# Kernel optimization log

Measured on AMD Instinct MI355X. Metric: run time of the kernel, lower is better.

The kernel has to match this reference:

```python
import jax, jax.numpy as jnp
import numpy as np

B = 512          # number of (query, corpus) pairs
MAX_SET = 128    # max_set_size
D_IN, E_IN = 32, 16
D = 128          # node_state_dim == filters_3
E_ENC = 64
M_HID = 256
T_DIM = 128      # transform_dim
N_PROP = 5
SINKHORN_ITERS = 20
TEMP = 0.1
DEG = 8


def setup_inputs() -> dict:
    key = jax.random.key(0)
    ks = jax.random.split(key, 16)
    # alternating graph sizes: query 128/64, corpus 64/128
    qsizes = np.where(np.arange(B) % 2 == 0, 128, 64).astype(np.int32)
    csizes = np.where(np.arange(B) % 2 == 0, 64, 128).astype(np.int32)
    sizes_flat = np.stack([qsizes, csizes], 1).reshape(-1)        # [2B] interleaved q,c
    N = int(sizes_flat.sum())                                     # 98304
    E = DEG * N                                                   # 786432
    starts = np.concatenate([[0], np.cumsum(sizes_flat)[:-1]])
    graph_idx = np.repeat(np.arange(2 * B), sizes_flat).astype(np.int32)
    rng = np.random.default_rng(0)
    from_idx = rng.integers(0, N, E).astype(np.int64)
    g = graph_idx[from_idx]                                       # keep edges within a graph
    to_idx = (starts[g] + rng.integers(0, 1 << 30, E) % sizes_flat[g]).astype(np.int64)

    def W(k, shape):
        s = 1.0 / np.sqrt(shape[0])
        return jax.random.uniform(k, shape, jnp.float32, -s, s)

    return dict(
        node_features=jax.random.normal(ks[0], (N, D_IN), jnp.float32),
        edge_features=jax.random.normal(ks[1], (E, E_IN), jnp.float32),
        enc_node_w=W(ks[2], (D_IN, D)), enc_node_b=jnp.zeros((D,), jnp.float32),
        enc_edge_w=W(ks[3], (E_IN, E_ENC)), enc_edge_b=jnp.zeros((E_ENC,), jnp.float32),
        msg_w1=W(ks[4], (2 * D + E_ENC, M_HID)), msg_b1=jnp.zeros((M_HID,), jnp.float32),
        msg_w2=W(ks[5], (M_HID, D)), msg_b2=jnp.zeros((D,), jnp.float32),
        rmsg_w1=W(ks[6], (2 * D + E_ENC, M_HID)), rmsg_b1=jnp.zeros((M_HID,), jnp.float32),
        rmsg_w2=W(ks[7], (M_HID, D)), rmsg_b2=jnp.zeros((D,), jnp.float32),
        upd_w1=W(ks[8], (2 * D, M_HID)), upd_b1=jnp.zeros((M_HID,), jnp.float32),
        upd_w2=W(ks[9], (M_HID, D)), upd_b2=jnp.zeros((D,), jnp.float32),
        fc1_w=W(ks[10], (D, T_DIM)), fc1_b=jnp.zeros((T_DIM,), jnp.float32),
        fc2_w=W(ks[11], (T_DIM, T_DIM)), fc2_b=jnp.zeros((T_DIM,), jnp.float32),
        from_idx=jnp.asarray(from_idx, jnp.int32),
        to_idx=jnp.asarray(to_idx, jnp.int32),
        graph_idx=jnp.asarray(graph_idx, jnp.int32),
        qsizes=jnp.asarray(qsizes, jnp.int32),
        csizes=jnp.asarray(csizes, jnp.int32),
    )


def _mlp2(x, w1, b1, w2, b2):
    return jax.nn.relu(x @ w1 + b1) @ w2 + b2


def reference(node_features, edge_features, enc_node_w, enc_node_b, enc_edge_w, enc_edge_b,
              msg_w1, msg_b1, msg_w2, msg_b2, rmsg_w1, rmsg_b1, rmsg_w2, rmsg_b2,
              upd_w1, upd_b1, upd_w2, upd_b2, fc1_w, fc1_b, fc2_w, fc2_b,
              from_idx, to_idx, graph_idx, qsizes, csizes):
    N = node_features.shape[0]
    # GraphEncoder: linear MLPs on node / edge features
    h = node_features @ enc_node_w + enc_node_b                   # [N, D]
    e = edge_features @ enc_edge_w + enc_edge_b                   # [E, E_ENC]
    # GraphPropLayer applied n_prop_layers times (shared params)
    for _ in range(N_PROP):
        src, dst = h[from_idx], h[to_idx]
        m = _mlp2(jnp.concatenate([src, dst, e], -1), msg_w1, msg_b1, msg_w2, msg_b2)
        agg = jax.ops.segment_sum(m, to_idx, num_segments=N)
        mr = _mlp2(jnp.concatenate([dst, src, e], -1), rmsg_w1, rmsg_b1, rmsg_w2, rmsg_b2)
        agg = agg + jax.ops.segment_sum(mr, from_idx, num_segments=N)
        h = h + _mlp2(jnp.concatenate([agg, h], -1), upd_w1, upd_b1, upd_w2, upd_b2)
    # split into per-graph chunks and pad to MAX_SET (scatter by (pair, side, position))
    sizes_flat = jnp.stack([qsizes, csizes], 1).reshape(-1)       # [2B]
    starts = jnp.concatenate([jnp.zeros((1,), sizes_flat.dtype), jnp.cumsum(sizes_flat)[:-1]])
    pos = jnp.arange(N, dtype=jnp.int32) - starts[graph_idx]
    pair, side = graph_idx // 2, graph_idx % 2
    stacked = jnp.zeros((B, 2, MAX_SET, D), h.dtype).at[pair, side, pos].set(h)
    stacked_q, stacked_c = stacked[:, 0], stacked[:, 1]           # [B, MAX_SET, D]
    # masked transform
    tq = _mlp2(stacked_q, fc1_w, fc1_b, fc2_w, fc2_b)
    tc = _mlp2(stacked_c, fc1_w, fc1_b, fc2_w, fc2_b)
    ar = jnp.arange(MAX_SET)
    qmask = (ar[None, :] < qsizes[:, None]).astype(h.dtype)[:, :, None]
    cmask = (ar[None, :] < csizes[:, None]).astype(h.dtype)[:, :, None]
    mq, mc = qmask * tq, cmask * tc
    # sinkhorn (noise_factor = 0, temperature = 0.1, 20 iters)
    log_alpha = jnp.einsum('bqd,bcd->bqc', mq, mc) / TEMP         # [B, MAX_SET, MAX_SET]
    for _ in range(SINKHORN_ITERS):
        log_alpha = log_alpha - jax.scipy.special.logsumexp(log_alpha, axis=2, keepdims=True)
        log_alpha = log_alpha - jax.scipy.special.logsumexp(log_alpha, axis=1, keepdims=True)
    plan = jnp.exp(log_alpha)
    # masked residual score
    scores = -jnp.sum(jax.nn.relu(stacked_q - plan @ stacked_c), axis=(1, 2))  # [B]
    return scores
```

## Files before the change

kernel.cpp:

```cpp
#include <hip/hip_runtime.h>

using bf16x8 = __attribute__((ext_vector_type(8))) __bf16;
using u16x8  = __attribute__((ext_vector_type(8))) unsigned short;
using f32x4  = __attribute__((ext_vector_type(4))) float;
using f32x2  = __attribute__((ext_vector_type(2))) float;

#define DEV static __device__ __forceinline__

constexpr int NN = 98304;
constexpr int NE = 786432;
constexpr int NB = 512;

constexpr size_t OFF_HB  = 0;
constexpr size_t OFF_AGG = OFF_HB + (size_t)NN*128*2;
constexpr size_t OFF_TH  = OFF_AGG;
constexpr size_t OFF_TL  = OFF_AGG + (size_t)NN*128*2;
constexpr size_t OFF_W   = OFF_AGG + (size_t)NN*128*4;

constexpr size_t WO_W1TM = 0;
constexpr size_t WO_W1TR = WO_W1TM + (size_t)81920*2;
constexpr size_t WO_W2TM = WO_W1TR + (size_t)81920*2;
constexpr size_t WO_W2TR = WO_W2TM + (size_t)32768*2;
constexpr size_t WO_W1TU = WO_W2TR + (size_t)32768*2;
constexpr size_t WO_W2TU = WO_W1TU + (size_t)65536*2;
constexpr size_t WO_WNT  = WO_W2TU + (size_t)32768*2;
constexpr size_t WO_WETP = WO_WNT  + (size_t)4096*2;
constexpr size_t WO_FC1F = WO_WETP + (size_t)2048*2;
constexpr size_t WO_FC2F = WO_FC1F + (size_t)16384*4;
constexpr size_t WO_BNF  = WO_FC2F + (size_t)16384*4;
constexpr size_t WO_BEF  = WO_BNF + 128*4;
constexpr size_t WO_B1M  = WO_BEF + 64*4;
constexpr size_t WO_B2M  = WO_B1M + 256*4;
constexpr size_t WO_B1R  = WO_B2M + 128*4;
constexpr size_t WO_B2R  = WO_B1R + 256*4;
constexpr size_t WO_B1U  = WO_B2R + 128*4;
constexpr size_t WO_B2U  = WO_B1U + 256*4;
constexpr size_t WO_FC1B = WO_B2U + 128*4;
constexpr size_t WO_FC2B = WO_FC1B + 128*4;
constexpr size_t WO_FLAG = WO_FC2B + 128*4;
constexpr size_t WO_END  = WO_FLAG + 16;

constexpr size_t OFF_HL  = OFF_W + WO_END;
constexpr size_t WS_MINI = OFF_HL;
constexpr size_t WS_FULL = OFF_HL + (size_t)NN*128*2;

constexpr int    SCAN_CHUNKS= NN/256;
constexpr size_t CSR_INTS   = (size_t)2*(NN+1) + (size_t)2*NN + (size_t)2*NE + 768;
constexpr size_t CSR_BYTES  = CSR_INTS*4;
constexpr size_t WS_FULL_G  = WS_FULL + CSR_BYTES;
constexpr size_t WS_MINI_G  = WS_MINI + CSR_BYTES;

DEV unsigned short f2bf(float f){
  unsigned u = __float_as_uint(f);
  u += 0x7fffu + ((u >> 16) & 1u);
  return (unsigned short)(u >> 16);
}
DEV float bf2f(unsigned short s){ return __uint_as_float(((unsigned)s) << 16); }

DEV unsigned short ldbf(const void* p, size_t i, int fl){
  return fl ? ((const unsigned short*)p)[i] : f2bf(((const float*)p)[i]);
}
DEV float ldf(const void* p, size_t i, int fl){
  return fl ? bf2f(((const unsigned short*)p)[i]) : ((const float*)p)[i];
}

DEV f32x4 mfma16(u16x8 a, u16x8 b, f32x4 c){
  bf16x8 A, B;
  __builtin_memcpy(&A, &a, 16);
  __builtin_memcpy(&B, &b, 16);
  return __builtin_amdgcn_mfma_f32_16x16x32_bf16(A, B, c, 0, 0, 0);
}

__global__ void k_dtype(const unsigned short* nf_u16, int* flag){
  if (threadIdx.x != 0 || blockIdx.x != 0) return;
  int sane = 0;
  for (int i = 0; i < 64; ++i){
    unsigned short v = nf_u16[2*i];
    int e = (v >> 7) & 0xFF;
    if (e >= 0x70 && e <= 0x8E) sane++;
  }
  *flag = (sane >= 32) ? 1 : 0;
}

__global__ void k_sent(float* out){
  int i = blockIdx.x*256 + threadIdx.x;
  if (i < NB) out[i] = 10000.f;
}

__global__ void k_canary(void* out, const int* flag){
  int i = blockIdx.x*256 + threadIdx.x;
  if (i < NB){
    if (*flag) ((unsigned short*)out)[i] = (unsigned short)0x4580u;
    else       ((float*)out)[i] = 4096.f;
  }
}

__global__ void k_zero(float* agg){
  f32x4* p = (f32x4*)agg;
  int gtid = blockIdx.x*256 + threadIdx.x;
  for (int i = gtid; i < NN*128/4; i += 786432){
    f32x4 z = {0.f, 0.f, 0.f, 0.f};
    p[i] = z;
  }
}

__global__ void k_prep(
  const void* enc_node_w, const void* enc_node_b,
  const void* enc_edge_w, const void* enc_edge_b,
  const void* msg_w1, const void* msg_b1,
  const void* msg_w2, const void* msg_b2,
  const void* rmsg_w1, const void* rmsg_b1,
  const void* rmsg_w2, const void* rmsg_b2,
  const void* upd_w1, const void* upd_b1,
  const void* upd_w2, const void* upd_b2,
  const void* fc1_w, const void* fc1_b,
  const void* fc2_w, const void* fc2_b,
  char* wsb)
{
  int fl = *(const int*)(wsb + OFF_W + WO_FLAG);
  int i = blockIdx.x*256 + threadIdx.x;
  unsigned short* W1Tm = (unsigned short*)(wsb + OFF_W + WO_W1TM);
  unsigned short* W1Tr = (unsigned short*)(wsb + OFF_W + WO_W1TR);
  unsigned short* W2Tm = (unsigned short*)(wsb + OFF_W + WO_W2TM);
  unsigned short* W2Tr = (unsigned short*)(wsb + OFF_W + WO_W2TR);
  unsigned short* W1Tu = (unsigned short*)(wsb + OFF_W + WO_W1TU);
  unsigned short* W2Tu = (unsigned short*)(wsb + OFF_W + WO_W2TU);
  unsigned short* WnT  = (unsigned short*)(wsb + OFF_W + WO_WNT);
  unsigned short* WeTp = (unsigned short*)(wsb + OFF_W + WO_WETP);
  float* fc1f = (float*)(wsb + OFF_W + WO_FC1F);
  float* fc2f = (float*)(wsb + OFF_W + WO_FC2F);
  float* bnf  = (float*)(wsb + OFF_W + WO_BNF);
  float* bef  = (float*)(wsb + OFF_W + WO_BEF);
  float* b1m  = (float*)(wsb + OFF_W + WO_B1M);
// ... 12 lines not shown
  if (i < 65536){ W1Tu[i] = ldbf(upd_w1,  (size_t)(i%256)*256 + (i/256), fl); return; } i -= 65536;
  if (i < 32768){ W2Tu[i] = ldbf(upd_w2,  (size_t)(i%256)*128 + (i/256), fl); return; } i -= 32768;
  if (i <  4096){ WnT[i]  = ldbf(enc_node_w, (size_t)(i%32)*128 + (i/32), fl); return; } i -= 4096;
  if (i <  2048){ int k = i%32, n = i/32;
                  WeTp[i] = (k<16) ? ldbf(enc_edge_w, (size_t)k*64 + n, fl) : (unsigned short)0; return; } i -= 2048;
  if (i < 16384){ fc1f[i] = ldf(fc1_w, i, fl); return; } i -= 16384;
  if (i < 16384){ fc2f[i] = ldf(fc2_w, i, fl); return; } i -= 16384;
  if (i <   128){ bnf[i] = ldf(enc_node_b, i, fl); return; } i -= 128;
  if (i <    64){ bef[i] = ldf(enc_edge_b, i, fl); return; } i -= 64;
  if (i <   256){ b1m[i] = ldf(msg_b1, i, fl); return; } i -= 256;
  if (i <   128){ b2m[i] = ldf(msg_b2, i, fl); return; } i -= 128;
  if (i <   256){ b1r[i] = ldf(rmsg_b1, i, fl); return; } i -= 256;
  if (i <   128){ b2r[i] = ldf(rmsg_b2, i, fl); return; } i -= 128;
  if (i <   256){ b1u[i] = ldf(upd_b1, i, fl); return; } i -= 256;
  if (i <   128){ b2u[i] = ldf(upd_b2, i, fl); return; } i -= 128;
  if (i <   128){ f1b[i] = ldf(fc1_b, i, fl); return; } i -= 128;
  if (i <   128){ f2b[i] = ldf(fc2_b, i, fl); return; }
}

__global__ void k_csr_zero(int* cur0, int* cur1){
  int i = blockIdx.x*256 + threadIdx.x;
  if (i < NN){ cur0[i] = 0; cur1[i] = 0; }
}
__global__ void k_csr_count(const int* from_idx, const int* to_idx, int* cur0, int* cur1){
  int e = blockIdx.x*256 + threadIdx.x;
  if (e < NE){
    atomicAdd(&cur0[to_idx[e]], 1);
    atomicAdd(&cur1[from_idx[e]], 1);
  }
}
__global__ void k_scan1(const int* cur0, const int* cur1, int* csum){
  __shared__ int red[256];
  int b = blockIdx.x, tid = threadIdx.x;
  const int* c = (b >= SCAN_CHUNKS) ? cur1 : cur0;
  int cb = (b >= SCAN_CHUNKS) ? (b - SCAN_CHUNKS) : b;
  red[tid] = c[cb*256 + tid];
  __syncthreads();
  for (int off = 128; off > 0; off >>= 1){
    if (tid < off) red[tid] += red[tid + off];
    __syncthreads();
  }
  if (tid == 0) csum[b] = red[0];
}
__global__ void k_scan2(int* csum, int* offs0, int* offs1){
  int wv = threadIdx.x >> 6, lane = threadIdx.x & 63;
  if (wv >= 2) return;
  int basei = wv * SCAN_CHUNKS;
  int carry = 0;
  for (int j = 0; j < SCAN_CHUNKS/64; ++j){
    int x = csum[basei + j*64 + lane];
    int s = x;
    for (int off = 1; off < 64; off <<= 1){
      int t = __shfl_up(s, off, 64);
      if (lane >= off) s += t;
    }
    csum[basei + j*64 + lane] = s - x + carry;
    carry += __shfl(s, 63, 64);
  }
  if (lane == 0){
    if (wv == 0) offs0[NN] = carry; else offs1[NN] = carry;
  }
}
__global__ void k_scan3(int* cur0, int* cur1, const int* csum, int* offs0, int* offs1){
  __shared__ int s[256];
  int b = blockIdx.x, tid = threadIdx.x;
  int dir = (b >= SCAN_CHUNKS) ? 1 : 0;
  int cb  = dir ? (b - SCAN_CHUNKS) : b;
  int* c    = dir ? cur1 : cur0;
  int* offs = dir ? offs1 : offs0;
  int v = c[cb*256 + tid];
  s[tid] = v;
  __syncthreads();
  for (int off = 1; off < 256; off <<= 1){
    int t = (tid >= off) ? s[tid - off] : 0;
    __syncthreads();
    s[tid] += t;
    __syncthreads();
  }
  int excl = s[tid] - v + csum[b];
  offs[cb*256 + tid] = excl;
  c[cb*256 + tid] = excl;
}
__global__ void k_csr_fill(const int* from_idx, const int* to_idx,
                           int* cur0, int* cur1, int* ent0, int* ent1){
  int e = blockIdx.x*256 + threadIdx.x;
  if (e < NE){
    int p0 = atomicAdd(&cur0[to_idx[e]], 1);   ent0[p0] = e;
    int p1 = atomicAdd(&cur1[from_idx[e]], 1); ent1[p1] = e;
  }
}

__global__ void __launch_bounds__(256) k_enc_node(
  const void* nf, const unsigned short* wnt, const float* bnf,
  unsigned short* hb, unsigned short* hl, int has_hl, const int* flag)
{
  int fl = *flag;
  const u16x8* wnt8 = (const u16x8*)wnt;
  int tid = threadIdx.x, wv = tid>>6, lane = tid&63, quad = lane>>4, l15 = lane&15;
  int n0 = blockIdx.x*64;
  f32x4 acc[4][2];
  for (int a=0;a<4;a++){ f32x4 z = {0.f,0.f,0.f,0.f}; acc[a][0]=z; acc[a][1]=z; }
  u16x8 av[4], bv[2];
  if (fl){
    const u16x8* nf8 = (const u16x8*)nf;
    for (int mt=0; mt<4; ++mt) av[mt] = nf8[(size_t)(n0 + mt*16 + l15)*4 + quad];
  } else {
    const float* nff = (const float*)nf;
    for (int mt=0; mt<4; ++mt){
      const float* rp = nff + (size_t)(n0 + mt*16 + l15)*32 + quad*8;
      u16x8 v;
      for (int j=0;j<8;j++) v[j] = f2bf(rp[j]);
      av[mt] = v;
    }
  }
  for (int nt=0; nt<2; ++nt) bv[nt] = wnt8[(size_t)(wv*32 + nt*16 + l15)*4 + quad];
  for (int mt=0; mt<4; ++mt)
    for (int nt=0; nt<2; ++nt)
      acc[mt][nt] = mfma16(av[mt], bv[nt], acc[mt][nt]);
  for (int mt=0; mt<4; ++mt)
    for (int nt=0; nt<2; ++nt){
      int n = wv*32 + nt*16 + l15;
      float bias = bnf[n];
      for (int r=0;r<4;r++){
        int m = mt*16 + quad*4 + r;
        float v = acc[mt][nt][r] + bias;
        size_t idx = (size_t)(n0+m)*128 + n;
        unsigned short hi = f2bf(v);
        hb[idx] = hi;
        if (has_hl) hl[idx] = f2bf(v - bf2f(hi));
      }
    }
}

__global__ void __launch_bounds__(256) k_msg(
  const unsigned short* hbg, const void* efg,
  const int* from_idx, const int* to_idx,
  const unsigned short* w1tm, const unsigned short* w1tr,
  const unsigned short* w2tm, const unsigned short* w2tr,
  const unsigned short* wetp, const float* bef,
  const float* b1m, const float* b2m, const float* b1r, const float* b2r,
  float* agg, const int* flag)
{
  __shared__ __align__(16) unsigned short XsB[40*32*8];
  __shared__ __align__(16) unsigned short HsB[32*32*8];
  __shared__ int fromS[32], toS[32];
  int fl = *flag;
  u16x8* Xs = (u16x8*)XsB;
  u16x8* Hs = (u16x8*)HsB;
  const u16x8* hb8   = (const u16x8*)hbg;
  const u16x8* wetp8 = (const u16x8*)wetp;
  const u16x8* w1tm8 = (const u16x8*)w1tm;
  const u16x8* w1tr8 = (const u16x8*)w1tr;
  const u16x8* w2tm8 = (const u16x8*)w2tm;
  const u16x8* w2tr8 = (const u16x8*)w2tr;

  int tid = threadIdx.x;
  int e0 = blockIdx.x*32;
  if (tid < 32) fromS[tid] = from_idx[e0 + tid];
  else if (tid < 64) toS[tid-32] = to_idx[e0 + tid - 32];
  __syncthreads();
  int m = tid & 31, g = tid >> 5;
  int wv = tid>>6, lane = tid&63, quad = lane>>4, l15 = lane&15;
  u16x8 zero8 = {0,0,0,0,0,0,0,0};

  for (int j=0; j<4; ++j){
    int kb = g + 8*j;
    u16x8 v = (kb < 16) ? hb8[(size_t)fromS[m]*16 + kb]
                        : hb8[(size_t)toS[m]*16 + (kb-16)];
    Xs[kb*32 + m] = v;
  }
// ... 93 lines not shown
  float* agg, const int* flag)
{
  __shared__ __align__(16) unsigned short XsB[40*64*8];
  __shared__ __align__(16) unsigned short HsB[32*64*8];
  __shared__ int eS[64], fromS[64], toS[64];
  __shared__ int runBeg[65];
  __shared__ int nRunsS;
  int fl = *flag;
  u16x8* Xs = (u16x8*)XsB;
  u16x8* Hs = (u16x8*)HsB;
  const u16x8* hb8   = (const u16x8*)hbg;
  const u16x8* wetp8 = (const u16x8*)wetp;
  const u16x8* w1tm8 = (const u16x8*)w1tm;
  const u16x8* w1tr8 = (const u16x8*)w1tr;
  const u16x8* w2tm8 = (const u16x8*)w2tm;
  const u16x8* w2tr8 = (const u16x8*)w2tr;

  int tid = threadIdx.x;
  int cpx = (int)gridDim.x >> 3;
  int bb = ((int)blockIdx.x & 7) * cpx + ((int)blockIdx.x >> 3);
  int e0 = bb * 64;
  if (tid < 64){
    int e = ent[e0 + tid];
    eS[tid] = e;
    fromS[tid] = from_idx[e];
    toS[tid]   = to_idx[e];
  }
  __syncthreads();
  int w = tid>>6, lane = tid&63, quad = lane>>4, l15 = lane&15;
  u16x8 zero8 = {0,0,0,0,0,0,0,0};

  if (tid == 0){
    int nr = 0;
    for (int mm=0; mm<64; ++mm)
      if (mm==0 || toS[mm]!=toS[mm-1]) runBeg[nr++] = mm;
    runBeg[nr] = 64; nRunsS = nr;
  }
  {
    int edge = tid & 63, cg = tid >> 6;
    for (int j=0; j<4; ++j){
      int kb = cg + 8*j;
      u16x8 v = (kb < 16) ? hb8[(size_t)fromS[edge]*16 + kb]
                          : hb8[(size_t)toS[edge]*16 + (kb-16)];
      Xs[kb*64 + edge] = v;
    }
  }
  {
    int wm = w >> 2, wn = w & 3;
    f32x4 accE[2];
    for (int a=0;a<2;a++){ f32x4 z = {0.f,0.f,0.f,0.f}; accE[a]=z; }
    u16x8 bvE = wetp8[(size_t)(wn*16 + l15)*4 + quad];
    for (int mt=0; mt<2; ++mt){
      u16x8 avE = zero8;
      if (quad < 2){
        int e = eS[wm*32 + mt*16 + l15];
        if (fl){
          avE = ((const u16x8*)efg)[(size_t)e*2 + quad];
        } else {
          const float* ep = (const float*)efg + (size_t)e*16 + quad*8;
          u16x8 v;
          for (int j=0;j<8;j++) v[j] = f2bf(ep[j]);
          avE = v;
        }
      }
      accE[mt] = mfma16(avE, bvE, accE[mt]);
    }
    int n = wn*16 + l15;
    float bias = bef[n];
    for (int mt=0; mt<2; ++mt)
      for (int r=0;r<4;r++){
        int me = wm*32 + mt*16 + quad*4 + r;
        XsB[((32 + (n>>3))*64 + me)*8 + (n&7)] = f2bf(accE[mt][r] + bias);
      }
  }
  __syncthreads();

  for (int dir=0; dir<2; ++dir){
    const u16x8* W1T = dir ? w1tr8 : w1tm8;
    const u16x8* W2T = dir ? w2tr8 : w2tm8;
    const float* B1  = dir ? b1r : b1m;
    f32x4 acc1[4][2];
    for (int a=0;a<4;a++)
      for (int b=0;b<2;b++){ f32x4 z = {0.f,0.f,0.f,0.f}; acc1[a][b]=z; }
    u16x8 bvA[2], bvB[2];
    for (int nt=0; nt<2; ++nt)
      bvA[nt] = W1T[(size_t)(w*32 + nt*16 + l15)*40 + quad];
    for (int ks=0; ks<10; ++ks){
      if (ks < 9)
        for (int nt=0; nt<2; ++nt)
          bvB[nt] = W1T[(size_t)(w*32 + nt*16 + l15)*40 + (ks+1)*4 + quad];
      else { bvB[0] = bvA[0]; bvB[1] = bvA[1]; }
      int kb = ks*4 + quad;
      int kbm = dir ? (kb < 32 ? (kb ^ 16) : kb) : kb;
      u16x8 av[4];
      for (int mt=0; mt<4; ++mt)
        av[mt] = Xs[kbm*64 + mt*16 + l15];
      for (int mt=0; mt<4; ++mt)
        for (int nt=0; nt<2; ++nt)
          acc1[mt][nt] = mfma16(av[mt], bvA[nt], acc1[mt][nt]);
      bvA[0] = bvB[0]; bvA[1] = bvB[1];
    }
    if (dir == 1) __syncthreads();
    for (int mt=0; mt<4; ++mt)
      for (int nt=0; nt<2; ++nt){
        int n = w*32 + nt*16 + l15;
        float bias = B1[n];
        for (int r=0;r<4;r++){
          int mm = mt*16 + quad*4 + r;
          float v = fmaxf(acc1[mt][nt][r] + bias, 0.f);
          HsB[((n>>3)*64 + mm)*8 + (n&7)] = f2bf(v);
        }
      }
    __syncthreads();
    f32x4 acc2[4];
    for (int a=0;a<4;a++){ f32x4 z = {0.f,0.f,0.f,0.f}; acc2[a]=z; }
    int n2 = w*16 + l15;
    u16x8 bvC = W2T[(size_t)n2*32 + quad];
    for (int ks=0; ks<8; ++ks){
      u16x8 bvN = bvC;
      if (ks < 7) bvN = W2T[(size_t)n2*32 + (ks+1)*4 + quad];
      u16x8 av[4];
      for (int mt=0; mt<4; ++mt)
        av[mt] = Hs[(ks*4 + quad)*64 + mt*16 + l15];
      for (int mt=0; mt<4; ++mt)
        acc2[mt] = mfma16(av[mt], bvC, acc2[mt]);
      bvC = bvN;
    }
    if (dir == 0){
      __syncthreads();
      float* P = (float*)HsB;
      float bias = b2m[n2];
      for (int mt=0; mt<4; ++mt)
        for (int r=0;r<4;r++){
          int mm = mt*16 + quad*4 + r;
          P[mm*128 + n2] = acc2[mt][r] + bias;
        }
      __syncthreads();
      int col = tid & 127, grp = tid >> 7;
      int nr = nRunsS;
      for (int k = grp; k < nr; k += 4){
        int r0 = runBeg[k], r1 = runBeg[k+1];
        float s = 0.f;
        for (int mm = r0; mm < r1; ++mm) s += P[mm*128 + col];
        atomicAdd(agg + (size_t)toS[r0]*128 + col, s);
      }
    } else {
      float bias = b2r[n2];
      for (int mt=0; mt<4; ++mt)
        for (int r=0;r<4;r++){
          int mm = mt*16 + quad*4 + r;
          atomicAdd(agg + (size_t)fromS[mm]*128 + n2, acc2[mt][r] + bias);
        }
    }
  }
}

__global__ void __launch_bounds__(512, 4) k_upd(
  float* agg, const unsigned short* hbg,
  const unsigned short* w1tu, const unsigned short* w2tu,
  const float* b1u, const float* b2u,
  unsigned short* hb, unsigned short* hl, int has_hl)
{
  __shared__ __align__(16) unsigned short XsB[32*64*8];
  __shared__ __align__(16) unsigned short HsB[32*64*8];
  u16x8* Xs = (u16x8*)XsB;
  u16x8* Hs = (u16x8*)HsB;
  const u16x8* hb8   = (const u16x8*)hbg;
  const u16x8* w1tu8 = (const u16x8*)w1tu;
  const u16x8* w2tu8 = (const u16x8*)w2tu;
  int tid = threadIdx.x;
  int n0 = blockIdx.x*64;
  {
    int node = tid & 63, cg = tid >> 6;
    for (int j=0; j<4; ++j){
      int kb = cg + 8*j;
      u16x8 v;
      if (kb < 16){
        const float* ap = agg + (size_t)(n0+node)*128 + kb*8;
        for (int t=0;t<8;t++) v[t] = f2bf(ap[t]);
      } else {
        v = hb8[(size_t)(n0+node)*16 + (kb-16)];
      }
      Xs[kb*64 + node] = v;
    }
  }
  __syncthreads();
  {
    f32x4* ap4 = (f32x4*)(agg + (size_t)n0*128);
    f32x4 z = {0.f,0.f,0.f,0.f};
    for (int i = tid; i < 64*128/4; i += 512) ap4[i] = z;
  }
  int w = tid>>6, lane = tid&63, quad = lane>>4, l15 = lane&15;
  f32x4 acc1[4][2];
  for (int a=0;a<4;a++)
    for (int b=0;b<2;b++){ f32x4 z = {0.f,0.f,0.f,0.f}; acc1[a][b]=z; }
  {
    u16x8 bvA[2], bvB[2];
    for (int nt=0; nt<2; ++nt)
      bvA[nt] = w1tu8[(size_t)(w*32 + nt*16 + l15)*32 + quad];
    for (int ks=0; ks<8; ++ks){
      if (ks < 7)
        for (int nt=0; nt<2; ++nt)
          bvB[nt] = w1tu8[(size_t)(w*32 + nt*16 + l15)*32 + (ks+1)*4 + quad];
      else { bvB[0] = bvA[0]; bvB[1] = bvA[1]; }
      u16x8 av[4];
      for (int mt=0; mt<4; ++mt)
        av[mt] = Xs[(ks*4 + quad)*64 + mt*16 + l15];
      for (int mt=0; mt<4; ++mt)
        for (int nt=0; nt<2; ++nt)
          acc1[mt][nt] = mfma16(av[mt], bvA[nt], acc1[mt][nt]);
      bvA[0] = bvB[0]; bvA[1] = bvB[1];
    }
  }
  __syncthreads();
  for (int mt=0; mt<4; ++mt)
    for (int nt=0; nt<2; ++nt){
      int n = w*32 + nt*16 + l15;
      float bias = b1u[n];
      for (int r=0;r<4;r++){
        int mm = mt*16 + quad*4 + r;
        float v = fmaxf(acc1[mt][nt][r] + bias, 0.f);
        HsB[((n>>3)*64 + mm)*8 + (n&7)] = f2bf(v);
      }
    }
  __syncthreads();
  f32x4 acc2[4];
  for (int a=0;a<4;a++){ f32x4 z = {0.f,0.f,0.f,0.f}; acc2[a]=z; }
  int n2 = w*16 + l15;
  {
    u16x8 bvC = w2tu8[(size_t)n2*32 + quad];
    for (int ks=0; ks<8; ++ks){
      u16x8 bvN = bvC;
      if (ks < 7) bvN = w2tu8[(size_t)n2*32 + (ks+1)*4 + quad];
      u16x8 av[4];
      for (int mt=0; mt<4; ++mt)
        av[mt] = Hs[(ks*4 + quad)*64 + mt*16 + l15];
      for (int mt=0; mt<4; ++mt)
        acc2[mt] = mfma16(av[mt], bvC, acc2[mt]);
      bvC = bvN;
    }
  }
  float bias = b2u[n2];
  for (int mt=0; mt<4; ++mt)
    for (int r=0;r<4;r++){
      int mm = mt*16 + quad*4 + r;
      size_t idx = (size_t)(n0+mm)*128 + n2;
      float base = bf2f(hb[idx]);
      if (has_hl) base += bf2f(hl[idx]);
      float nv = base + acc2[mt][r] + bias;
      unsigned short hi = f2bf(nv);
      hb[idx] = hi;
      if (has_hl) hl[idx] = f2bf(nv - bf2f(hi));
    }
}

__global__ void __launch_bounds__(256) k_tmlp(
  const unsigned short* hb, const unsigned short* hl, int has_hl,
  const float* fc1f, const float* fc2f,
  const float* fc1b, const float* fc2b, unsigned short* Th, unsigned short* Tl)
{
  __shared__ float Xs[16][128];
  __shared__ float Hsm[16][128];
  int tid = threadIdx.x, wv = tid>>6, lane = tid&63;
  int nodeBase = blockIdx.x*16 + wv*4;
  for (int i=0;i<4;i++){
    size_t base = (size_t)(nodeBase+i)*128 + lane*2;
    float x0 = bf2f(hb[base]), x1 = bf2f(hb[base+1]);
    if (has_hl){ x0 += bf2f(hl[base]); x1 += bf2f(hl[base+1]); }
    Xs[wv*4+i][lane*2] = x0; Xs[wv*4+i][lane*2+1] = x1;
  }
  __syncthreads();
  float a0[4], a1[4];
  for (int i=0;i<4;i++){ a0[i] = fc1b[lane*2]; a1[i] = fc1b[lane*2+1]; }
  for (int k=0;k<128;k++){
    f32x2 w = *(const f32x2*)&fc1f[k*128 + lane*2];
    for (int i=0;i<4;i++){ float x = Xs[wv*4+i][k]; a0[i] += x*w[0]; a1[i] += x*w[1]; }
  }
  for (int i=0;i<4;i++){
    Hsm[wv*4+i][lane*2]   = fmaxf(a0[i], 0.f);
    Hsm[wv*4+i][lane*2+1] = fmaxf(a1[i], 0.f);
  }
  __syncthreads();
  for (int i=0;i<4;i++){ a0[i] = fc2b[lane*2]; a1[i] = fc2b[lane*2+1]; }
  for (int k=0;k<128;k++){
    f32x2 w = *(const f32x2*)&fc2f[k*128 + lane*2];
    for (int i=0;i<4;i++){ float x = Hsm[wv*4+i][k]; a0[i] += x*w[0]; a1[i] += x*w[1]; }
  }
  for (int i=0;i<4;i++){
    size_t idx = (size_t)(nodeBase+i)*128 + lane*2;
    float t0 = a0[i], t1 = a1[i];
    unsigned short h0 = f2bf(t0), h1 = f2bf(t1);
    Th[idx] = h0; Th[idx+1] = h1;
    Tl[idx]   = f2bf(t0 - bf2f(h0));
    Tl[idx+1] = f2bf(t1 - bf2f(h1));
  }
}

__global__ void __launch_bounds__(256) k_pair(
  const unsigned short* Th, const unsigned short* Tl,
  const unsigned short* hb, const unsigned short* hl, int has_hl,
  void* outv, const int* flag)
{
  __shared__ float la[8448];
  __shared__ float red[4];
  const u16x8* th8 = (const u16x8*)Th;
  const u16x8* tl8 = (const u16x8*)Tl;
  int b = blockIdx.x;
  int even = ((b & 1) == 0);
  int qs = even ? 128 : 64;
  int cs = 192 - qs;
  int nr = even ? 128 : 65;
  int nc = even ? 65 : 128;
  int st = nc + 1;
  int q0 = 192*b, c0 = q0 + qs;
  int tid = threadIdx.x, wv = tid>>6, lane = tid&63, quad = lane>>4, l15 = lane&15;
  u16x8 zero8 = {0,0,0,0,0,0,0,0};

  f32x4 acc[2][8];
  for (int a=0;a<2;a++)
    for (int c=0;c<8;c++){ f32x4 z = {0.f,0.f,0.f,0.f}; acc[a][c]=z; }
  for (int pass=0; pass<3; ++pass){
    const u16x8* A  = (pass==2) ? tl8 : th8;
    const u16x8* Bm = (pass==1) ? tl8 : th8;
// ... 16 lines not shown
    for (int nt=0; nt<8; ++nt)
      for (int r=0;r<4;r++){
        int q = wv*32 + mt*16 + quad*4 + r;
        int c = nt*16 + l15;
        if (q < nr && c < nc) la[q*st + c] = acc[mt][nt][r] * 10.0f;
      }
  __syncthreads();

  for (int it=0; it<20; ++it){
    if (tid < nr){
      float* row = &la[tid*st];
      float mx = -1e30f;
      for (int c=0;c<nc;c++) mx = fmaxf(mx, row[c]);
      float s = 0.f, last = 0.f;
      for (int c=0;c<nc;c++){ float e = __expf(row[c]-mx); s += e; last = e; }
      if (even) s += 63.f * last;
      float l = mx + __logf(s);
      for (int c=0;c<nc;c++) row[c] -= l;
    }
    __syncthreads();
    if (tid < nc){
      int c = tid;
      float mx = -1e30f;
      for (int r=0;r<nr;r++) mx = fmaxf(mx, la[r*st + c]);
      float s = 0.f, last = 0.f;
      for (int r=0;r<nr;r++){ float e = __expf(la[r*st + c]-mx); s += e; last = e; }
      if (!even) s += 63.f * last;
      float l = mx + __logf(s);
      for (int r=0;r<nr;r++) la[r*st + c] -= l;
    }
    __syncthreads();
  }
  for (int i = tid; i < 8448; i += 256) la[i] = __expf(la[i]);
  __syncthreads();

  int d = tid & 127, qg = tid >> 7;
  int nsweep = (nr + 15) >> 4;
  float partial = 0.f;
  for (int sweep=0; sweep<nsweep; ++sweep){
    int qb = sweep*16 + qg*8;
    float acc2[8];
    for (int j=0;j<8;j++) acc2[j] = 0.f;
    for (int c=0; c<cs; ++c){
      size_t si = (size_t)(c0+c)*128 + d;
      float s = bf2f(hb[si]);
      if (has_hl) s += bf2f(hl[si]);
      for (int j=0;j<8;j++){
        int r = qb + j;
        if (r < nr) acc2[j] += la[r*st + c] * s;
      }
    }
    for (int j=0;j<8;j++){
      int r = qb + j;
      if (r < nr){
        float w = (!even && r == 64) ? 64.f : 1.f;
        float sq = 0.f;
        if (r < qs){
          size_t si = (size_t)(q0+r)*128 + d;
          sq = bf2f(hb[si]);
          if (has_hl) sq += bf2f(hl[si]);
        }
        partial += w * fmaxf(sq - acc2[j], 0.f);
      }
    }
  }
  for (int off=32; off>0; off>>=1) partial += __shfl_down(partial, off, 64);
  if (lane == 0) red[wv] = partial;
  __syncthreads();
  if (tid == 0){
    float tot = red[0] + red[1] + red[2] + red[3];
    if (*flag) ((unsigned short*)outv)[b] = f2bf(-tot);
    else       ((float*)outv)[b] = -tot;
  }
}

extern "C" void kernel_launch(void* const* d_in, const int* in_sizes, int n_in,
                              void* d_out, int out_size, void* d_ws, size_t ws_size,
                              hipStream_t stream)
{
  if (ws_size < WS_MINI){
    k_sent<<<2, 256, 0, stream>>>((float*)d_out);
    return;
  }
  int has_hl = 0, use_s8 = 0;
  size_t off_csr = 0;
  if (ws_size >= WS_FULL_G){ has_hl = 1; use_s8 = 1; off_csr = WS_FULL; }
  else if (ws_size >= WS_FULL){ has_hl = 1; use_s8 = 0; }
  else if (ws_size >= WS_MINI_G){ has_hl = 0; use_s8 = 1; off_csr = WS_MINI; }

  const int* from_idx = (const int*)d_in[22];
  const int* to_idx   = (const int*)d_in[23];

  char* wsb = (char*)d_ws;
  unsigned short* hb  = (unsigned short*)(wsb + OFF_HB);
  unsigned short* hl  = (unsigned short*)(wsb + OFF_HL);
  float* agg          = (float*)(wsb + OFF_AGG);
  unsigned short* Th  = (unsigned short*)(wsb + OFF_TH);
  unsigned short* Tl  = (unsigned short*)(wsb + OFF_TL);
  int* flag           = (int*)(wsb + OFF_W + WO_FLAG);

  const unsigned short* w1tm = (const unsigned short*)(wsb + OFF_W + WO_W1TM);
  const unsigned short* w1tr = (const unsigned short*)(wsb + OFF_W + WO_W1TR);
  const unsigned short* w2tm = (const unsigned short*)(wsb + OFF_W + WO_W2TM);
  const unsigned short* w2tr = (const unsigned short*)(wsb + OFF_W + WO_W2TR);
  const unsigned short* w1tu = (const unsigned short*)(wsb + OFF_W + WO_W1TU);
  const unsigned short* w2tu = (const unsigned short*)(wsb + OFF_W + WO_W2TU);
  const unsigned short* wnt  = (const unsigned short*)(wsb + OFF_W + WO_WNT);
  const unsigned short* wetp = (const unsigned short*)(wsb + OFF_W + WO_WETP);
  const float* fc1f  = (const float*)(wsb + OFF_W + WO_FC1F);
  const float* fc2f  = (const float*)(wsb + OFF_W + WO_FC2F);
  const float* bnf   = (const float*)(wsb + OFF_W + WO_BNF);
  const float* bef   = (const float*)(wsb + OFF_W + WO_BEF);
  const float* b1m   = (const float*)(wsb + OFF_W + WO_B1M);
  const float* b2m   = (const float*)(wsb + OFF_W + WO_B2M);
  const float* b1r   = (const float*)(wsb + OFF_W + WO_B1R);
  const float* b2r   = (const float*)(wsb + OFF_W + WO_B2R);
  const float* b1u   = (const float*)(wsb + OFF_W + WO_B1U);
  const float* b2u   = (const float*)(wsb + OFF_W + WO_B2U);
  const float* f1b   = (const float*)(wsb + OFF_W + WO_FC1B);
  const float* f2b   = (const float*)(wsb + OFF_W + WO_FC2B);

  int* offs0 = (int*)(wsb + off_csr);
  int* offs1 = offs0 + (NN + 1);
  int* cur0  = offs1 + (NN + 1);
  int* cur1  = cur0 + NN;
  int* ent0  = cur1 + NN;
  int* ent1  = ent0 + NE;
  int* csum  = ent1 + NE;

  k_dtype<<<1, 64, 0, stream>>>((const unsigned short*)d_in[0], flag);

  k_canary<<<2, 256, 0, stream>>>(d_out, flag);

  k_prep<<<1439, 256, 0, stream>>>(
    d_in[2],  d_in[3],  d_in[4],  d_in[5],
    d_in[6],  d_in[7],  d_in[8],  d_in[9],
    d_in[10], d_in[11], d_in[12], d_in[13],
    d_in[14], d_in[15], d_in[16], d_in[17],
    d_in[18], d_in[19], d_in[20], d_in[21],
    wsb);

  if (use_s8){
    k_csr_zero <<<NN/256, 256, 0, stream>>>(cur0, cur1);
    k_csr_count<<<NE/256, 256, 0, stream>>>(from_idx, to_idx, cur0, cur1);
    k_scan1    <<<2*SCAN_CHUNKS, 256, 0, stream>>>(cur0, cur1, csum);
    k_scan2    <<<1, 128, 0, stream>>>(csum, offs0, offs1);
    k_scan3    <<<2*SCAN_CHUNKS, 256, 0, stream>>>(cur0, cur1, csum, offs0, offs1);
    k_csr_fill <<<NE/256, 256, 0, stream>>>(from_idx, to_idx, cur0, cur1, ent0, ent1);
  }

  k_enc_node<<<NN/64, 256, 0, stream>>>(d_in[0], wnt, bnf, hb, hl, has_hl, flag);

  k_zero<<<3072, 256, 0, stream>>>(agg);
  for (int r=0; r<5; ++r){
    if (use_s8){
      k_msg8<<<NE/64, 512, 0, stream>>>(hb, d_in[1],
          from_idx, to_idx, ent0, w1tm, w1tr, w2tm, w2tr, wetp, bef,
          b1m, b2m, b1r, b2r, agg, flag);
    } else {
      k_msg<<<NE/32, 256, 0, stream>>>(hb, d_in[1],
          from_idx, to_idx, w1tm, w1tr, w2tm, w2tr, wetp, bef,
          b1m, b2m, b1r, b2r, agg, flag);
    }
    k_upd<<<NN/64, 512, 0, stream>>>(agg, hb, w1tu, w2tu, b1u, b2u, hb, hl, has_hl);
  }

  k_tmlp<<<NN/16, 256, 0, stream>>>(hb, hl, has_hl, fc1f, fc2f, f1b, f2b, Th, Tl);
  k_pair<<<NB, 256, 0, stream>>>(Th, Tl, hb, hl, has_hl, d_out, flag);
}
```

Baseline: 5.816 ms.

## Replace reverse-message atomic scatter with buffered bf16 messages gathered via CSR

Adds a path in which the reverse-direction edge messages are no longer atomically added to random source-node rows. Instead they are written as bf16 rows into a per-edge buffer, and a new update kernel gathers them per node through the from-index CSR plus an inverse permutation built during CSR fill. The goal is to cut the contention and traffic of roughly a hundred million float atomics per round. The cost is a large extra workspace plus a bf16 rounding of each message before summation. It also drops the software double-buffered weight prefetch in the message and update GEMM loops. The path only runs when the workspace is big enough.

```diff
diff --git a/kernel.cpp b/kernel.cpp
--- a/kernel.cpp
+++ b/kernel.cpp
@@ -49,6 +49,10 @@
 constexpr size_t CSR_BYTES  = CSR_INTS*4;
 constexpr size_t WS_FULL_G  = WS_FULL + CSR_BYTES;
 constexpr size_t WS_MINI_G  = WS_MINI + CSR_BYTES;
+
+constexpr size_t OFF_INV0 = WS_FULL_G;
+constexpr size_t OFF_M1   = OFF_INV0 + (size_t)NE*4;
+constexpr size_t WS_G2    = OFF_M1 + (size_t)NE*128*2;
 
 DEV unsigned short f2bf(float f){
   unsigned u = __float_as_uint(f);
@@ -227,10 +231,11 @@
   c[cb*256 + tid] = excl;
 }
 __global__ void k_csr_fill(const int* from_idx, const int* to_idx,
-                           int* cur0, int* cur1, int* ent0, int* ent1){
+                           int* cur0, int* cur1, int* ent0, int* ent1, int* inv0){
   int e = blockIdx.x*256 + threadIdx.x;
   if (e < NE){
     int p0 = atomicAdd(&cur0[to_idx[e]], 1);   ent0[p0] = e;
+    if (inv0) inv0[e] = p0;
     int p1 = atomicAdd(&cur1[from_idx[e]], 1); ent1[p1] = e;
   }
 }
@@ -490,23 +495,17 @@
     f32x4 acc1[4][2];
     for (int a=0;a<4;a++)
       for (int b=0;b<2;b++){ f32x4 z = {0.f,0.f,0.f,0.f}; acc1[a][b]=z; }
-    u16x8 bvA[2], bvB[2];
-    for (int nt=0; nt<2; ++nt)
-      bvA[nt] = W1T[(size_t)(w*32 + nt*16 + l15)*40 + quad];
     for (int ks=0; ks<10; ++ks){
-      if (ks < 9)
-        for (int nt=0; nt<2; ++nt)
-          bvB[nt] = W1T[(size_t)(w*32 + nt*16 + l15)*40 + (ks+1)*4 + quad];
-      else { bvB[0] = bvA[0]; bvB[1] = bvA[1]; }
+      u16x8 bv[2], av[4];
+      for (int nt=0; nt<2; ++nt)
+        bv[nt] = W1T[(size_t)(w*32 + nt*16 + l15)*40 + ks*4 + quad];
       int kb = ks*4 + quad;
       int kbm = dir ? (kb < 32 ? (kb ^ 16) : kb) : kb;
-      u16x8 av[4];
       for (int mt=0; mt<4; ++mt)
         av[mt] = Xs[kbm*64 + mt*16 + l15];
       for (int mt=0; mt<4; ++mt)
         for (int nt=0; nt<2; ++nt)
-          acc1[mt][nt] = mfma16(av[mt], bvA[nt], acc1[mt][nt]);
-      bvA[0] = bvB[0]; bvA[1] = bvB[1];
+          acc1[mt][nt] = mfma16(av[mt], bv[nt], acc1[mt][nt]);
     }
     if (dir == 1) __syncthreads();
     for (int mt=0; mt<4; ++mt)
@@ -523,16 +522,13 @@
     f32x4 acc2[4];
     for (int a=0;a<4;a++){ f32x4 z = {0.f,0.f,0.f,0.f}; acc2[a]=z; }
     int n2 = w*16 + l15;
-    u16x8 bvC = W2T[(size_t)n2*32 + quad];
     for (int ks=0; ks<8; ++ks){
-      u16x8 bvN = bvC;
-      if (ks < 7) bvN = W2T[(size_t)n2*32 + (ks+1)*4 + quad];
+      u16x8 bv1 = W2T[(size_t)n2*32 + ks*4 + quad];
       u16x8 av[4];
       for (int mt=0; mt<4; ++mt)
         av[mt] = Hs[(ks*4 + quad)*64 + mt*16 + l15];
       for (int mt=0; mt<4; ++mt)
-        acc2[mt] = mfma16(av[mt], bvC, acc2[mt]);
-      bvC = bvN;
+        acc2[mt] = mfma16(av[mt], bv1, acc2[mt]);
     }
     if (dir == 0){
       __syncthreads();
@@ -559,6 +555,158 @@
           int mm = mt*16 + quad*4 + r;
           atomicAdd(agg + (size_t)fromS[mm]*128 + n2, acc2[mt][r] + bias);
         }
+    }
+  }
+}
+
+__global__ void __launch_bounds__(512, 4) k_msg10(
+  const unsigned short* hbg, const void* efg,
+  const int* from_idx, const int* to_idx, const int* ent,
+  const unsigned short* w1tm, const unsigned short* w1tr,
+  const unsigned short* w2tm, const unsigned short* w2tr,
+  const unsigned short* wetp, const float* bef,
+  const float* b1m, const float* b2m, const float* b1r, const float* b2r,
+  float* agg, unsigned short* m1, const int* flag)
+{
+  __shared__ __align__(16) unsigned short XsB[40*64*8];
+  __shared__ __align__(16) unsigned short HsB[32*64*8];
+  __shared__ int eS[64], fromS[64], toS[64];
+  __shared__ int runBeg[65];
+  __shared__ int nRunsS;
+  int fl = *flag;
+  u16x8* Xs = (u16x8*)XsB;
+  u16x8* Hs = (u16x8*)HsB;
+  const u16x8* hb8   = (const u16x8*)hbg;
+  const u16x8* wetp8 = (const u16x8*)wetp;
+  const u16x8* w1tm8 = (const u16x8*)w1tm;
+  const u16x8* w1tr8 = (const u16x8*)w1tr;
+  const u16x8* w2tm8 = (const u16x8*)w2tm;
+  const u16x8* w2tr8 = (const u16x8*)w2tr;
+
+  int tid = threadIdx.x;
+  int cpx = (int)gridDim.x >> 3;
+  int bb = ((int)blockIdx.x & 7) * cpx + ((int)blockIdx.x >> 3);
+  int e0 = bb * 64;
+  if (tid < 64){
+    int e = ent[e0 + tid];
+    eS[tid] = e;
+    fromS[tid] = from_idx[e];
+    toS[tid]   = to_idx[e];
+  }
+  __syncthreads();
+  int w = tid>>6, lane = tid&63, quad = lane>>4, l15 = lane&15;
+  u16x8 zero8 = {0,0,0,0,0,0,0,0};
+
+  if (tid == 0){
+    int nr = 0;
+    for (int mm=0; mm<64; ++mm)
+      if (mm==0 || toS[mm]!=toS[mm-1]) runBeg[nr++] = mm;
+    runBeg[nr] = 64; nRunsS = nr;
+  }
+  {
+    int edge = tid & 63, cg = tid >> 6;
+    for (int j=0; j<4; ++j){
+      int kb = cg + 8*j;
+      u16x8 v = (kb < 16) ? hb8[(size_t)fromS[edge]*16 + kb]
+                          : hb8[(size_t)toS[edge]*16 + (kb-16)];
+      Xs[kb*64 + edge] = v;
+    }
+  }
+  {
+    int wm = w >> 2, wn = w & 3;
+    f32x4 accE[2];
+    for (int a=0;a<2;a++){ f32x4 z = {0.f,0.f,0.f,0.f}; accE[a]=z; }
+    u16x8 bvE = wetp8[(size_t)(wn*16 + l15)*4 + quad];
+    for (int mt=0; mt<2; ++mt){
+      u16x8 avE = zero8;
+      if (quad < 2){
+        int e = eS[wm*32 + mt*16 + l15];
+        if (fl){
+          avE = ((const u16x8*)efg)[(size_t)e*2 + quad];
+        } else {
+          const float* ep = (const float*)efg + (size_t)e*16 + quad*8;
+          u16x8 v;
+          for (int j=0;j<8;j++) v[j] = f2bf(ep[j]);
+          avE = v;
+        }
+      }
+      accE[mt] = mfma16(avE, bvE, accE[mt]);
+    }
+    int n = wn*16 + l15;
+    float bias = bef[n];
+    for (int mt=0; mt<2; ++mt)
+      for (int r=0;r<4;r++){
+        int me = wm*32 + mt*16 + quad*4 + r;
+        XsB[((32 + (n>>3))*64 + me)*8 + (n&7)] = f2bf(accE[mt][r] + bias);
+      }
+  }
+  __syncthreads();
+
+  for (int dir=0; dir<2; ++dir){
+    const u16x8* W1T = dir ? w1tr8 : w1tm8;
+    const u16x8* W2T = dir ? w2tr8 : w2tm8;
+    const float* B1  = dir ? b1r : b1m;
+    f32x4 acc1[4][2];
+    for (int a=0;a<4;a++)
+      for (int b=0;b<2;b++){ f32x4 z = {0.f,0.f,0.f,0.f}; acc1[a][b]=z; }
+    for (int ks=0; ks<10; ++ks){
+      u16x8 bv[2], av[4];
+      for (int nt=0; nt<2; ++nt)
+        bv[nt] = W1T[(size_t)(w*32 + nt*16 + l15)*40 + ks*4 + quad];
+      int kb = ks*4 + quad;
+      int kbm = dir ? (kb < 32 ? (kb ^ 16) : kb) : kb;
+      for (int mt=0; mt<4; ++mt)
+        av[mt] = Xs[kbm*64 + mt*16 + l15];
+      for (int mt=0; mt<4; ++mt)
+        for (int nt=0; nt<2; ++nt)
+          acc1[mt][nt] = mfma16(av[mt], bv[nt], acc1[mt][nt]);
+    }
+    if (dir == 1) __syncthreads();
+    for (int mt=0; mt<4; ++mt)
+      for (int nt=0; nt<2; ++nt){
+        int n = w*32 + nt*16 + l15;
+        float bias = B1[n];
+        for (int r=0;r<4;r++){
+          int mm = mt*16 + quad*4 + r;
+          float v = fmaxf(acc1[mt][nt][r] + bias, 0.f);
+          HsB[((n>>3)*64 + mm)*8 + (n&7)] = f2bf(v);
+        }
+      }
+    __syncthreads();
+    f32x4 acc2[4];
+    for (int a=0;a<4;a++){ f32x4 z = {0.f,0.f,0.f,0.f}; acc2[a]=z; }
+    int n2 = w*16 + l15;
+    for (int ks=0; ks<8; ++ks){
+      u16x8 bv1 = W2T[(size_t)n2*32 + ks*4 + quad];
+      u16x8 av[4];
+      for (int mt=0; mt<4; ++mt)
+        av[mt] = Hs[(ks*4 + quad)*64 + mt*16 + l15];
+      for (int mt=0; mt<4; ++mt)
+        acc2[mt] = mfma16(av[mt], bv1, acc2[mt]);
+    }
+    __syncthreads();
+    float* P = (float*)HsB;
+    {
+      float bias = dir ? b2r[n2] : b2m[n2];
+      for (int mt=0; mt<4; ++mt)
+        for (int r=0;r<4;r++){
+          int mm = mt*16 + quad*4 + r;
+          P[mm*128 + n2] = acc2[mt][r] + bias;
+        }
+    }
+    __syncthreads();
+    if (dir == 0){
+      int col = tid & 127, grp = tid >> 7;
+      int nr = nRunsS;
+      for (int k = grp; k < nr; k += 4){
+        int r0 = runBeg[k], r1 = runBeg[k+1];
+        float s = 0.f;
+        for (int mm = r0; mm < r1; ++mm) s += P[mm*128 + col];
+        atomicAdd(agg + (size_t)toS[r0]*128 + col, s);
+      }
+    } else {
+      for (int i = tid; i < 64*128; i += 512)
+        m1[(size_t)(e0 + (i >> 7))*128 + (i & 127)] = f2bf(P[i]);
     }
   }
 }
@@ -602,23 +750,15 @@
   f32x4 acc1[4][2];
   for (int a=0;a<4;a++)
     for (int b=0;b<2;b++){ f32x4 z = {0.f,0.f,0.f,0.f}; acc1[a][b]=z; }
-  {
-    u16x8 bvA[2], bvB[2];
+  for (int ks=0; ks<8; ++ks){
+    u16x8 bv[2], av[4];
     for (int nt=0; nt<2; ++nt)
-      bvA[nt] = w1tu8[(size_t)(w*32 + nt*16 + l15)*32 + quad];
-    for (int ks=0; ks<8; ++ks){
-      if (ks < 7)
-        for (int nt=0; nt<2; ++nt)
-          bvB[nt] = w1tu8[(size_t)(w*32 + nt*16 + l15)*32 + (ks+1)*4 + quad];
-      else { bvB[0] = bvA[0]; bvB[1] = bvA[1]; }
-      u16x8 av[4];
-      for (int mt=0; mt<4; ++mt)
-        av[mt] = Xs[(ks*4 + quad)*64 + mt*16 + l15];
-      for (int mt=0; mt<4; ++mt)
-        for (int nt=0; nt<2; ++nt)
-          acc1[mt][nt] = mfma16(av[mt], bvA[nt], acc1[mt][nt]);
-      bvA[0] = bvB[0]; bvA[1] = bvB[1];
-    }
+      bv[nt] = w1tu8[(size_t)(w*32 + nt*16 + l15)*32 + ks*4 + quad];
+    for (int mt=0; mt<4; ++mt)
+      av[mt] = Xs[(ks*4 + quad)*64 + mt*16 + l15];
+    for (int mt=0; mt<4; ++mt)
+      for (int nt=0; nt<2; ++nt)
+        acc1[mt][nt] = mfma16(av[mt], bv[nt], acc1[mt][nt]);
   }
   __syncthreads();
   for (int mt=0; mt<4; ++mt)
@@ -635,18 +775,111 @@
   f32x4 acc2[4];
   for (int a=0;a<4;a++){ f32x4 z = {0.f,0.f,0.f,0.f}; acc2[a]=z; }
   int n2 = w*16 + l15;
+  for (int ks=0; ks<8; ++ks){
+    u16x8 bv2 = w2tu8[(size_t)n2*32 + ks*4 + quad];
+    u16x8 av[4];
+    for (int mt=0; mt<4; ++mt)
+      av[mt] = Hs[(ks*4 + quad)*64 + mt*16 + l15];
+    for (int mt=0; mt<4; ++mt)
+      acc2[mt] = mfma16(av[mt], bv2, acc2[mt]);
+  }
+  float bias = b2u[n2];
+  for (int mt=0; mt<4; ++mt)
+    for (int r=0;r<4;r++){
+      int mm = mt*16 + quad*4 + r;
+      size_t idx = (size_t)(n0+mm)*128 + n2;
+      float base = bf2f(hb[idx]);
+      if (has_hl) base += bf2f(hl[idx]);
+      float nv = base + acc2[mt][r] + bias;
+      unsigned short hi = f2bf(nv);
+      hb[idx] = hi;
+      if (has_hl) hl[idx] = f2bf(nv - bf2f(hi));
+    }
+}
+
+__global__ void __launch_bounds__(512, 4) k_upd2(
+  float* agg, const unsigned short* m1, const int* ent1, const int* inv0,
+  const int* offs1, const unsigned short* hbg,
+  const unsigned short* w1tu, const unsigned short* w2tu,
+  const float* b1u, const float* b2u,
+  unsigned short* hb, unsigned short* hl, int has_hl)
+{
+  __shared__ __align__(16) unsigned short XsB[32*64*8];
+  __shared__ __align__(16) unsigned short HsB[32*64*8];
+  u16x8* Xs = (u16x8*)XsB;
+  u16x8* Hs = (u16x8*)HsB;
+  const u16x8* hb8   = (const u16x8*)hbg;
+  const u16x8* m18   = (const u16x8*)m1;
+  const u16x8* w1tu8 = (const u16x8*)w1tu;
+  const u16x8* w2tu8 = (const u16x8*)w2tu;
+  int tid = threadIdx.x;
+  int n0 = blockIdx.x*64;
   {
-    u16x8 bvC = w2tu8[(size_t)n2*32 + quad];
-    for (int ks=0; ks<8; ++ks){
-      u16x8 bvN = bvC;
-      if (ks < 7) bvN = w2tu8[(size_t)n2*32 + (ks+1)*4 + quad];
-      u16x8 av[4];
-      for (int mt=0; mt<4; ++mt)
-        av[mt] = Hs[(ks*4 + quad)*64 + mt*16 + l15];
-      for (int mt=0; mt<4; ++mt)
-        acc2[mt] = mfma16(av[mt], bvC, acc2[mt]);
-      bvC = bvN;
-    }
+    int node = tid >> 3, chunk = tid & 7;
+    float a[16];
+    const f32x4* ap = (const f32x4*)(agg + (size_t)(n0+node)*128 + chunk*16);
+    for (int q=0;q<4;q++){ f32x4 v = ap[q]; a[q*4]=v[0]; a[q*4+1]=v[1]; a[q*4+2]=v[2]; a[q*4+3]=v[3]; }
+    int jb = offs1[n0+node], je = offs1[n0+node+1];
+    for (int j = jb; j < je; ++j){
+      int s = inv0[ent1[j]];
+      u16x8 v0 = m18[(size_t)s*16 + chunk*2];
+      u16x8 v1 = m18[(size_t)s*16 + chunk*2 + 1];
+      for (int t=0;t<8;t++){ a[t] += bf2f(v0[t]); a[8+t] += bf2f(v1[t]); }
+    }
+    u16x8 o0, o1;
+    for (int t=0;t<8;t++){ o0[t] = f2bf(a[t]); o1[t] = f2bf(a[8+t]); }
+    Xs[(chunk*2)*64 + node]   = o0;
+    Xs[(chunk*2+1)*64 + node] = o1;
+  }
+  {
+    int node = tid & 63, cg = tid >> 6;
+    for (int j=0; j<2; ++j){
+      int kb = 16 + cg + 8*j;
+      Xs[kb*64 + node] = hb8[(size_t)(node + n0)*16 + (kb-16)];
+    }
+  }
+  __syncthreads();
+  {
+    f32x4* ap4 = (f32x4*)(agg + (size_t)n0*128);
+    f32x4 z = {0.f,0.f,0.f,0.f};
+    for (int i = tid; i < 64*128/4; i += 512) ap4[i] = z;
+  }
+  int w = tid>>6, lane = tid&63, quad = lane>>4, l15 = lane&15;
+  f32x4 acc1[4][2];
+  for (int a=0;a<4;a++)
+    for (int b=0;b<2;b++){ f32x4 z = {0.f,0.f,0.f,0.f}; acc1[a][b]=z; }
+  for (int ks=0; ks<8; ++ks){
+    u16x8 bv[2], av[4];
+    for (int nt=0; nt<2; ++nt)
+      bv[nt] = w1tu8[(size_t)(w*32 + nt*16 + l15)*32 + ks*4 + quad];
+    for (int mt=0; mt<4; ++mt)
+      av[mt] = Xs[(ks*4 + quad)*64 + mt*16 + l15];
+    for (int mt=0; mt<4; ++mt)
+      for (int nt=0; nt<2; ++nt)
+        acc1[mt][nt] = mfma16(av[mt], bv[nt], acc1[mt][nt]);
+  }
+  __syncthreads();
+  for (int mt=0; mt<4; ++mt)
+    for (int nt=0; nt<2; ++nt){
+      int n = w*32 + nt*16 + l15;
+      float bias = b1u[n];
+      for (int r=0;r<4;r++){
+        int mm = mt*16 + quad*4 + r;
+        float v = fmaxf(acc1[mt][nt][r] + bias, 0.f);
+        HsB[((n>>3)*64 + mm)*8 + (n&7)] = f2bf(v);
+      }
+    }
+  __syncthreads();
+  f32x4 acc2[4];
+  for (int a=0;a<4;a++){ f32x4 z = {0.f,0.f,0.f,0.f}; acc2[a]=z; }
+  int n2 = w*16 + l15;
+  for (int ks=0; ks<8; ++ks){
+    u16x8 bv2 = w2tu8[(size_t)n2*32 + ks*4 + quad];
+    u16x8 av[4];
+    for (int mt=0; mt<4; ++mt)
+      av[mt] = Hs[(ks*4 + quad)*64 + mt*16 + l15];
+    for (int mt=0; mt<4; ++mt)
+      acc2[mt] = mfma16(av[mt], bv2, acc2[mt]);
   }
   float bias = b2u[n2];
   for (int mt=0; mt<4; ++mt)
@@ -829,9 +1062,10 @@
     k_sent<<<2, 256, 0, stream>>>((float*)d_out);
     return;
   }
-  int has_hl = 0, use_s8 = 0;
+  int has_hl = 0, use_s8 = 0, use_g2 = 0;
   size_t off_csr = 0;
-  if (ws_size >= WS_FULL_G){ has_hl = 1; use_s8 = 1; off_csr = WS_FULL; }
+  if (ws_size >= WS_G2){ has_hl = 1; use_s8 = 1; use_g2 = 1; off_csr = WS_FULL; }
+  else if (ws_size >= WS_FULL_G){ has_hl = 1; use_s8 = 1; off_csr = WS_FULL; }
   else if (ws_size >= WS_FULL){ has_hl = 1; use_s8 = 0; }
   else if (ws_size >= WS_MINI_G){ has_hl = 0; use_s8 = 1; off_csr = WS_MINI; }
 
@@ -874,6 +1108,8 @@
   int* ent0  = cur1 + NN;
   int* ent1  = ent0 + NE;
   int* csum  = ent1 + NE;
+  int* inv0  = use_g2 ? (int*)(wsb + OFF_INV0) : (int*)nullptr;
+  unsigned short* m1 = (unsigned short*)(wsb + OFF_M1);
 
   k_dtype<<<1, 64, 0, stream>>>((const unsigned short*)d_in[0], flag);
 
@@ -893,23 +1129,30 @@
     k_scan1    <<<2*SCAN_CHUNKS, 256, 0, stream>>>(cur0, cur1, csum);
     k_scan2    <<<1, 128, 0, stream>>>(csum, offs0, offs1);
     k_scan3    <<<2*SCAN_CHUNKS, 256, 0, stream>>>(cur0, cur1, csum, offs0, offs1);
-    k_csr_fill <<<NE/256, 256, 0, stream>>>(from_idx, to_idx, cur0, cur1, ent0, ent1);
+    k_csr_fill <<<NE/256, 256, 0, stream>>>(from_idx, to_idx, cur0, cur1, ent0, ent1, inv0);
   }
 
   k_enc_node<<<NN/64, 256, 0, stream>>>(d_in[0], wnt, bnf, hb, hl, has_hl, flag);
 
   k_zero<<<3072, 256, 0, stream>>>(agg);
   for (int r=0; r<5; ++r){
-    if (use_s8){
+    if (use_g2){
+      k_msg10<<<NE/64, 512, 0, stream>>>(hb, d_in[1],
+          from_idx, to_idx, ent0, w1tm, w1tr, w2tm, w2tr, wetp, bef,
+          b1m, b2m, b1r, b2r, agg, m1, flag);
+      k_upd2<<<NN/64, 512, 0, stream>>>(agg, m1, ent1, inv0, offs1,
+          hb, w1tu, w2tu, b1u, b2u, hb, hl, has_hl);
+    } else if (use_s8){
       k_msg8<<<NE/64, 512, 0, stream>>>(hb, d_in[1],
           from_idx, to_idx, ent0, w1tm, w1tr, w2tm, w2tr, wetp, bef,
           b1m, b2m, b1r, b2r, agg, flag);
+      k_upd<<<NN/64, 512, 0, stream>>>(agg, hb, w1tu, w2tu, b1u, b2u, hb, hl, has_hl);
     } else {
       k_msg<<<NE/32, 256, 0, stream>>>(hb, d_in[1],
           from_idx, to_idx, w1tm, w1tr, w2tm, w2tr, wetp, bef,
           b1m, b2m, b1r, b2r, agg, flag);
-    }
-    k_upd<<<NN/64, 512, 0, stream>>>(agg, hb, w1tu, w2tu, b1u, b2u, hb, hl, has_hl);
+      k_upd<<<NN/64, 512, 0, stream>>>(agg, hb, w1tu, w2tu, b1u, b2u, hb, hl, has_hl);
+    }
   }
 
   k_tmlp<<<NN/16, 256, 0, stream>>>(hb, hl, has_hl, fc1f, fc2f, f1b, f2b, Th, Tl);
```

After: 5.807 ms. No clear change (-0.1%).
